# Optimization experiments

Hardware: AMD Instinct MI355X
Metric: run time of the kernel (lower is better)

Reference implementation:

```python
import jax, jax.numpy as jnp
import numpy as np

CONF_THRESH = 0.01
TOP_K = 200
NMS_THRESH = 0.45


def setup_inputs() -> dict:
    key = jax.random.key(0)
    k1, k2, k3, k4, k5 = jax.random.split(key, 5)
    B, N, C = 32, 8732, 21
    return {
        "loc_data": jax.random.normal(k1, (B, N, 4), jnp.float32),
        "conf_data": jax.random.normal(k2, (B, N, C), jnp.float32),
        "loc_data2": jax.random.normal(k3, (B, N, 4), jnp.float32),
        "conf_data2": jax.random.normal(k4, (B, N, C), jnp.float32),
        "dbox_list": jax.random.uniform(k5, (N, 4), jnp.float32),
    }


def decode(loc, dbox):
    # SSD decode with variances (0.1, 0.2); loc,dbox: [N,4]; returns xyxy
    cxcy = dbox[:, :2] + loc[:, :2] * 0.1 * dbox[:, 2:]
    wh = dbox[:, 2:] * jnp.exp(loc[:, 2:] * 0.2)
    return jnp.concatenate([cxcy - wh * 0.5, cxcy + wh * 0.5], axis=-1)


def iou_matrix(b):
    # b: [K,4] xyxy -> [K,K] IoU
    x1 = jnp.maximum(b[:, None, 0], b[None, :, 0])
    y1 = jnp.maximum(b[:, None, 1], b[None, :, 1])
    x2 = jnp.minimum(b[:, None, 2], b[None, :, 2])
    y2 = jnp.minimum(b[:, None, 3], b[None, :, 3])
    inter = jnp.clip(x2 - x1, 0.0) * jnp.clip(y2 - y1, 0.0)
    area = (b[:, 2] - b[:, 0]) * (b[:, 3] - b[:, 1])
    union = area[:, None] + area[None, :] - inter
    return inter / union


def nms_class(scores, boxes):
    # scores: [M], boxes: [M,4] for one (image, class)
    masked = jnp.where(scores > CONF_THRESH, scores, -1.0)  # drop sub-threshold
    cand_s, idx = jax.lax.top_k(masked, TOP_K)              # top_k candidate pool
    cand_b = boxes[idx]
    valid = cand_s > CONF_THRESH
    iou = iou_matrix(cand_b)

    def step(suppressed, j):
        keep_j = valid[j] & (~suppressed[j])
        suppressed = suppressed | (keep_j & (iou[j] > NMS_THRESH))
        return suppressed, keep_j

    _, keep = jax.lax.scan(step, jnp.zeros((TOP_K,), bool), jnp.arange(TOP_K))
    entries = jnp.concatenate([cand_s[:, None], cand_b], axis=1)  # [K,5] = (score, box)
    pos = jnp.cumsum(keep) - 1
    pos = jnp.where(keep, pos, TOP_K)  # out-of-bounds -> dropped
    return jnp.zeros((TOP_K, 5), entries.dtype).at[pos].set(entries, mode="drop")


def reference(loc_data, conf_data, loc_data2, conf_data2, dbox_list):
    B, N, _ = loc_data.shape
    C = conf_data.shape[2]
    conf = jax.nn.softmax(conf_data, axis=-1)    # [B,N,C]
    conf2 = jax.nn.softmax(conf_data2, axis=-1)
    boxes1 = jax.vmap(decode, in_axes=(0, None))(loc_data, dbox_list)   # [B,N,4]
    boxes2 = jax.vmap(decode, in_axes=(0, None))(loc_data2, dbox_list)
    # horizontal flip of second (TTA) view: x1' = 1 - x2, x2' = 1 - x1
    boxes2 = jnp.stack(
        [1.0 - boxes2[..., 2], boxes2[..., 1], 1.0 - boxes2[..., 0], boxes2[..., 3]],
        axis=-1,
    )
    boxes = jnp.concatenate([boxes1, boxes2], axis=1)   # [B,2N,4]
    scores = jnp.concatenate([conf, conf2], axis=1)     # [B,2N,C]
    scores = jnp.moveaxis(scores, -1, 1)                # [B,C,2N]
    # vmap over batch and (non-background) classes
    per_class = jax.vmap(jax.vmap(nms_class, in_axes=(0, None)), in_axes=(0, 0))(
        scores[:, 1:], boxes
    )  # [B,C-1,TOP_K,5]
    out = jnp.zeros((B, C, TOP_K, 5), loc_data.dtype)
    return out.at[:, 1:].set(per_class)
```

## Files before the change

### kernel.cpp

```cpp
#include <hip/hip_runtime.h>

#define B_ 32
#define N_ 8732
#define N2_ 17464
#define N4_ 4366
#define C_ 21
#define NCLS 20
#define K_ 200
#define CONF_T 0.01f
#define NMS_T 0.45f
#define TPB_S 256
#define TPB_N 512
#define POOL 1024
#define RANKCAP 512
#define HB 1024

typedef unsigned long long u64;
typedef unsigned int u32;

__global__ __launch_bounds__(TPB_S) void softmax_kernel(
    const float* __restrict__ conf1, const float* __restrict__ conf2,
    float* __restrict__ scores)
{
  __shared__ float lds[TPB_S * C_];
  const int t = threadIdx.x;
  const int tile = blockIdx.x * TPB_S;
  const int b = blockIdx.y;
  const int view = blockIdx.z;
  int cnt = N_ - tile; if (cnt > TPB_S) cnt = TPB_S;
  const float* conf = view ? conf2 : conf1;
  const float4* src = (const float4*)(conf + ((size_t)b * N_ + tile) * C_);
  float4* l4 = (float4*)lds;
  const int n4 = (cnt * C_) >> 2;
  for (int i = t; i < n4; i += TPB_S) l4[i] = src[i];
  __syncthreads();
  if (t < cnt) {
    float x[C_];
#pragma unroll
    for (int i = 0; i < C_; ++i) x[i] = lds[t * C_ + i];
    float m = x[0];
#pragma unroll
    for (int i = 1; i < C_; ++i) m = fmaxf(m, x[i]);
    float e[C_];
    float sum = 0.0f;
#pragma unroll
    for (int i = 0; i < C_; ++i) { e[i] = __expf(x[i] - m); sum += e[i]; }
    float inv = 1.0f / sum;
    float* o = scores + ((size_t)b * NCLS) * N2_ + (size_t)view * N_ + (tile + t);
#pragma unroll
    for (int c = 1; c < C_; ++c) { *o = e[c] * inv; o += N2_; }
  }
}

__global__ __launch_bounds__(TPB_N, 2) void nms_kernel(
    const float* __restrict__ scores,
    const float4* __restrict__ loc1,
    const float4* __restrict__ loc2,
    const float4* __restrict__ dbox,
    float* __restrict__ out)
{
  const int t = threadIdx.x;
  const int lane = t & 63;
  const int wv = t >> 6;
  const int bimg = blockIdx.x / NCLS;
  const int cls = 1 + (blockIdx.x % NCLS);
  const float4* sc4 = (const float4*)(scores + ((size_t)bimg * NCLS + (cls - 1)) * N2_);
  float* ob = out + ((size_t)bimg * C_ + cls) * K_ * 5;

  __shared__ u32 hist[HB];
  __shared__ u64 pool[POOL] __attribute__((aligned(16)));
  __shared__ u64 spool[256];
  __shared__ float4 bb[K_];
  __shared__ float bar[K_];
  __shared__ u64 rowmask[K_][4];
  __shared__ u64 validmask[4];
  __shared__ u32 wtot[8];
  __shared__ u32 sh_sel, sh_Sb, sh_Sn, sh_nc;

  {
    const float4 z4 = make_float4(0.f, 0.f, 0.f, 0.f);
    if (t < 250) ((float4*)ob)[t] = z4;
    if (cls == 1 && t >= 256 && t < 506)
      ((float4*)(out + (size_t)bimg * C_ * K_ * 5))[t - 256] = z4;
  }

  float4 v[9];
#pragma unroll
  for (int k = 0; k < 9; ++k) {
    int i = t + k * TPB_N;
    v[k] = (i < N4_) ? sc4[i] : make_float4(0.f, 0.f, 0.f, 0.f);
  }

  hist[t] = 0u;
  pool[t] = 0ULL; pool[t + TPB_N] = 0ULL;
  if (t == 0) sh_nc = 0u;
  __syncthreads();

  {
    const int hb = wv << 6;
#pragma unroll
    for (int k = 0; k < 9; ++k) {
      float ss[4] = {v[k].x, v[k].y, v[k].z, v[k].w};
#pragma unroll
      for (int c2 = 0; c2 < 4; ++c2) {
        float s = ss[c2];
        if (s > CONF_T)
          atomicAdd(&hist[hb + ((__float_as_uint(s) >> 20) - 960u)], 1u);
      }
    }
  }
  __syncthreads();

  if (t < 64) {
    u32 c = hist[t]       + hist[t + 64]  + hist[t + 128] + hist[t + 192]
          + hist[t + 256] + hist[t + 320] + hist[t + 384] + hist[t + 448];
    u32 x = c;
#pragma unroll
    for (int off = 1; off < 64; off <<= 1) {
      u32 y = __shfl_down(x, off);
      if (lane + off < 64) x += y;
    }
    u32 total = __shfl(x, 0);
    u32 Sn = x - c;
    if (total < (u32)K_) {
      if (t == 0) sh_sel = 0xFFFFFFFFu;
    } else if (x >= (u32)K_ && Sn < (u32)K_) {
      sh_sel = (u32)t; sh_Sb = x; sh_Sn = Sn;
    }
  }
  __syncthreads();

  u32 loKey, prefix = 0, Gacc = 0;
  bool needMore = false;
  if (sh_sel == 0xFFFFFFFFu) {
    loKey = 1u;
  } else {
    prefix = sh_sel + 960u;
    loKey = prefix << 20;
    Gacc = sh_Sn;
    needMore = sh_Sb > (u32)RANKCAP;
  }

  for (int lvl = 1; lvl <= 2 && needMore; ++lvl) {
    const int shift = (lvl == 1) ? 10 : 0;
    const int mshift = shift + 10;
    for (int h = t; h < HB; h += TPB_N) hist[h] = 0u;
    __syncthreads();
#pragma unroll
    for (int k = 0; k < 9; ++k) {
      float ss[4] = {v[k].x, v[k].y, v[k].z, v[k].w};
#pragma unroll
      for (int c2 = 0; c2 < 4; ++c2) {
        float s = ss[c2];
        if (s > CONF_T) {
          u32 key = __float_as_uint(s);
          if ((key >> mshift) == prefix)
            atomicAdd(&hist[(key >> shift) & (HB - 1)], 1u);
        }
      }
    }
    __syncthreads();
    u32 c0 = hist[2 * t], c1 = hist[2 * t + 1];
    u32 T = c0 + c1;
    u32 x = T;
#pragma unroll
    for (int off = 1; off < 64; off <<= 1) {
      u32 y = __shfl_down(x, off);
      if (lane + off < 64) x += y;
    }
    if (lane == 0) wtot[wv] = x;
    __syncthreads();
    u32 wafter = 0;
    for (int w = wv + 1; w < 8; ++w) wafter += wtot[w];
    u32 after_me = (x - T) + wafter;
    u32 S1 = c1 + after_me, S0 = c0 + S1;
    hist[2 * t] = S0; hist[2 * t + 1] = S1;
    __syncthreads();
    u32 need = (u32)K_ - Gacc;
    for (int h = t; h < HB; h += TPB_N) {
      u32 Sb = hist[h];
      u32 Sn2 = (h + 1 < HB) ? hist[h + 1] : 0u;
      if (Sb >= need && Sn2 < need) { sh_sel = (u32)h; sh_Sb = Sb; sh_Sn = Sn2; }
    }
    __syncthreads();
    prefix = (prefix << 10) | sh_sel;
    u32 candTotal = Gacc + sh_Sb;
    Gacc += sh_Sn;
    loKey = prefix << shift;
    needMore = (candTotal > (u32)RANKCAP) && (lvl < 2);
  }

#pragma unroll
  for (int k = 0; k < 9; ++k) {
    int i = t + k * TPB_N;
    float ss[4] = {v[k].x, v[k].y, v[k].z, v[k].w};
#pragma unroll
    for (int c2 = 0; c2 < 4; ++c2) {
      float s = ss[c2];
      u32 key = __float_as_uint(s);
      bool pred = (s > CONF_T) && (key >= loKey);
      u64 bal = __ballot(pred);
      if (bal) {
        u32 wb = 0;
        if (lane == 0) wb = atomicAdd(&sh_nc, (u32)__popcll(bal));
        wb = __shfl(wb, 0);
        if (pred) {
          u32 pos = wb + (u32)__popcll(bal & ((1ULL << lane) - 1ULL));
          if (pos < (u32)POOL)
            pool[pos] = ((u64)key << 32) | (u64)(0xFFFFFFFFu - (u32)(i * 4 + c2));
        }
      }
    }
  }
  __syncthreads();

  u32 nc = sh_nc < (u32)POOL ? sh_nc : (u32)POOL;
  if (t < 256) spool[t] = 0ULL;
  const bool dual = nc > (u32)TPB_N;
  u64 my0 = (t < (int)nc) ? pool[t] : 0ULL;
  u64 my1 = (dual && t + TPB_N < (int)nc) ? pool[t + TPB_N] : 0ULL;
  __syncthreads();
  u32 r0 = 0, r1 = 0;
  if ((u32)(t & ~63) < nc) {
    if (!dual) {
#pragma unroll 4
      for (u32 k = 0; k < nc; k += 2) {
        ulonglong2 pk = *(const ulonglong2*)&pool[k];
        r0 += (pk.x > my0) ? 1u : 0u;
        r0 += (pk.y > my0) ? 1u : 0u;
      }
    } else {
#pragma unroll 4
      for (u32 k = 0; k < nc; k += 2) {
        ulonglong2 pk = *(const ulonglong2*)&pool[k];
        r0 += (pk.x > my0) ? 1u : 0u;
        r0 += (pk.y > my0) ? 1u : 0u;
        r1 += (pk.x > my1) ? 1u : 0u;
        r1 += (pk.y > my1) ? 1u : 0u;
      }
    }
  }
  if (my0 != 0ULL && r0 < (u32)K_) spool[r0] = my0;
  if (dual && my1 != 0ULL && r1 < (u32)K_) spool[r1] = my1;
  __syncthreads();

  float scv = 0.f;
  if (t < K_) {
    float x1 = 0.f, y1 = 0.f, x2 = 0.f, y2 = 0.f, area = 0.f;
    u64 e = spool[t];
    u32 kb = (u32)(e >> 32);
    if (kb != 0u) {
      scv = __uint_as_float(kb);
      u32 idx = 0xFFFFFFFFu - (u32)(e & 0xFFFFFFFFu);
      int nn = (idx < (u32)N_) ? (int)idx : (int)(idx - N_);
      float4 l = (idx < (u32)N_) ? loc1[(size_t)bimg * N_ + nn]
                                 : loc2[(size_t)bimg * N_ + nn];
      float4 d = dbox[nn];
      float cx = d.x + l.x * 0.1f * d.z;
      float cy = d.y + l.y * 0.1f * d.w;
      float w = d.z * __expf(l.z * 0.2f);
      float h = d.w * __expf(l.w * 0.2f);
      x1 = cx - w * 0.5f; y1 = cy - h * 0.5f;
      x2 = cx + w * 0.5f; y2 = cy + h * 0.5f;
      if (idx >= (u32)N_) {
        float tmp = 1.0f - x2; x2 = 1.0f - x1; x1 = tmp;
      }
      area = (x2 - x1) * (y2 - y1);
    }
    bb[t] = make_float4(x1, y1, x2, y2);
    bar[t] = area;
  } else if (t >= 256) {
    for (int i = t - 256; i < 4 * K_; i += 256) ((u64*)rowmask)[i] = 0ULL;
  }
  {
    bool myvalid = (t < K_) && (scv > CONF_T);
    u64 bal = __ballot(myvalid);
    if (lane == 0 && wv < 4) validmask[wv] = bal;
  }
  __syncthreads();

  if (t < 2 * K_) {
    const int j = (t < K_) ? t : (t - K_);
    const int h = (t < K_) ? 0 : 1;
    const int L = K_ - 1 - j;
    const int half = (L + 1) >> 1;
    const int s0c = j + 1 + (h ? half : 0);
    const int e0c = h ? K_ : (j + 1 + half);
    if (s0c < e0c) {
      float4 mb = bb[j];
      float ma = bar[j];
      for (int w = (s0c >> 6); w <= ((e0c - 1) >> 6); ++w) {
        int ka = (w << 6) > s0c ? (w << 6) : s0c;
        int kb2 = ((w + 1) << 6) < e0c ? ((w + 1) << 6) : e0c;
        u64 m = 0ULL;
        for (int k2 = ka; k2 < kb2; ++k2) {
          float4 obx = bb[k2];
          float ox1 = fmaxf(mb.x, obx.x);
          float oy1 = fmaxf(mb.y, obx.y);
          float ox2 = fminf(mb.z, obx.z);
          float oy2 = fminf(mb.w, obx.w);
          float inter = fmaxf(ox2 - ox1, 0.f) * fmaxf(oy2 - oy1, 0.f);
          float uni = ma + bar[k2] - inter;
          m |= (inter > NMS_T * uni) ? (1ULL << (k2 & 63)) : 0ULL;
        }
        if (m) atomicOr(&rowmask[j][w], m);
      }
    }
  }
  __syncthreads();

  if (t < 64) {
    const u64 vv0 = validmask[0], vv1 = validmask[1];
    const u64 vv2 = validmask[2], vv3 = validmask[3];
    u64 s0 = 0, s1 = 0, s2 = 0, s3 = 0;
    u64 k0 = 0, k1 = 0, k2m = 0, k3 = 0;
#pragma unroll 8
    for (int j = 0; j < 64; ++j) {
      u64 q0 = rowmask[j][0], q1 = rowmask[j][1], q2 = rowmask[j][2], q3 = rowmask[j][3];
      u64 bit = 1ULL << j;
      if ((vv0 & bit) && !(s0 & bit)) { s0 |= q0; s1 |= q1; s2 |= q2; s3 |= q3; k0 |= bit; }
    }
#pragma unroll 8
    for (int j = 64; j < 128; ++j) {
      u64 q1 = rowmask[j][1], q2 = rowmask[j][2], q3 = rowmask[j][3];
      u64 bit = 1ULL << (j & 63);
      if ((vv1 & bit) && !(s1 & bit)) { s1 |= q1; s2 |= q2; s3 |= q3; k1 |= bit; }
    }
#pragma unroll 8
    for (int j = 128; j < 192; ++j) {
      u64 q2 = rowmask[j][2], q3 = rowmask[j][3];
      u64 bit = 1ULL << (j & 63);
      if ((vv2 & bit) && !(s2 & bit)) { s2 |= q2; s3 |= q3; k2m |= bit; }
    }
#pragma unroll
    for (int j = 192; j < K_; ++j) {
      u64 q3 = rowmask[j][3];
      u64 bit = 1ULL << (j & 63);
      if ((vv3 & bit) && !(s3 & bit)) { s3 |= q3; k3 |= bit; }
    }
    const u32 n0 = (u32)__popcll(k0);
    const u32 n01 = n0 + (u32)__popcll(k1);
    const u32 n012 = n01 + (u32)__popcll(k2m);
    const u64 below = (1ULL << lane) - 1ULL;
#pragma unroll
    for (int w = 0; w < 4; ++w) {
      int j = (w << 6) + lane;
      if (j < K_) {
        u64 kw = (w == 0) ? k0 : (w == 1) ? k1 : (w == 2) ? k2m : k3;
        if ((kw >> lane) & 1ULL) {
          int pos2 = (int)__popcll(kw & below)
                  + (int)((w == 0) ? 0u : (w == 1) ? n0 : (w == 2) ? n01 : n012);
          u64 e = spool[j];
          float sc = __uint_as_float((u32)(e >> 32));
          float4 bx = bb[j];
          float* o = ob + (size_t)pos2 * 5;
          o[0] = sc; o[1] = bx.x; o[2] = bx.y; o[3] = bx.z; o[4] = bx.w;
        }
      }
    }
  }
}

extern "C" void kernel_launch(void* const* d_in, const int* in_sizes, int n_in,
                              void* d_out, int out_size, void* d_ws, size_t ws_size,
                              hipStream_t stream) {
  const float* loc1 = (const float*)d_in[0];
  const float* conf1 = (const float*)d_in[1];
  const float* loc2 = (const float*)d_in[2];
  const float* conf2 = (const float*)d_in[3];
  const float* dbox = (const float*)d_in[4];
  float* out = (float*)d_out;
  float* scores = (float*)d_ws;

  dim3 g1((N_ + TPB_S - 1) / TPB_S, B_, 2);
  softmax_kernel<<<g1, TPB_S, 0, stream>>>(conf1, conf2, scores);

  nms_kernel<<<B_ * NCLS, TPB_N, 0, stream>>>(
      scores, (const float4*)loc1, (const float4*)loc2, (const float4*)dbox, out);
}
```

Before: 157.0 us.

## Store softmax max/inv-sum only and recompute class scores inside NMS kernel

The first kernel now writes only a per-box (max, 1/sum) pair instead of the full 20-class transposed probability array. The NMS kernel reads the raw logits for its class with a stride of C, applies exp and scale itself, and uses the shared denominators. Blocks are reordered so consecutive blocks handle the same class across images, which changes the cache access pattern. This cuts the intermediate workspace write and read traffic, but NMS blocks now make strided, uncoalesced gathers and compute extra exps per element.

```diff
diff --git a/kernel.cpp b/kernel.cpp
--- a/kernel.cpp
+++ b/kernel.cpp
@@ -18,9 +18,9 @@
 typedef unsigned long long u64;
 typedef unsigned int u32;
 
-__global__ __launch_bounds__(TPB_S) void softmax_kernel(
+__global__ __launch_bounds__(TPB_S) void denom_kernel(
     const float* __restrict__ conf1, const float* __restrict__ conf2,
-    float* __restrict__ scores)
+    float2* __restrict__ denom)
 {
   __shared__ float lds[TPB_S * C_];
   const int t = threadIdx.x;
@@ -41,19 +41,18 @@
     float m = x[0];
 #pragma unroll
     for (int i = 1; i < C_; ++i) m = fmaxf(m, x[i]);
-    float e[C_];
     float sum = 0.0f;
 #pragma unroll
-    for (int i = 0; i < C_; ++i) { e[i] = __expf(x[i] - m); sum += e[i]; }
+    for (int i = 0; i < C_; ++i) sum += __expf(x[i] - m);
     float inv = 1.0f / sum;
-    float* o = scores + ((size_t)b * NCLS) * N2_ + (size_t)view * N_ + (tile + t);
-#pragma unroll
-    for (int c = 1; c < C_; ++c) { *o = e[c] * inv; o += N2_; }
+    denom[(size_t)b * N2_ + (size_t)view * N_ + tile + t] = make_float2(m, inv);
   }
 }
 
 __global__ __launch_bounds__(TPB_N, 2) void nms_kernel(
-    const float* __restrict__ scores,
+    const float* __restrict__ conf1,
+    const float* __restrict__ conf2,
+    const float2* __restrict__ denom,
     const float4* __restrict__ loc1,
     const float4* __restrict__ loc2,
     const float4* __restrict__ dbox,
@@ -62,9 +61,8 @@
   const int t = threadIdx.x;
   const int lane = t & 63;
   const int wv = t >> 6;
-  const int bimg = blockIdx.x / NCLS;
-  const int cls = 1 + (blockIdx.x % NCLS);
-  const float4* sc4 = (const float4*)(scores + ((size_t)bimg * NCLS + (cls - 1)) * N2_);
+  const int bimg = blockIdx.x & 31;
+  const int cls = 1 + (blockIdx.x >> 5);
   float* ob = out + ((size_t)bimg * C_ + cls) * K_ * 5;
 
   __shared__ u32 hist[HB];
@@ -88,7 +86,22 @@
 #pragma unroll
   for (int k = 0; k < 9; ++k) {
     int i = t + k * TPB_N;
-    v[k] = (i < N4_) ? sc4[i] : make_float4(0.f, 0.f, 0.f, 0.f);
+    if (i < N4_) {
+      const int a0 = i << 2;
+      const float* cb = (a0 < N_)
+        ? conf1 + ((size_t)bimg * N_ + a0) * C_ + cls
+        : conf2 + ((size_t)bimg * N_ + (a0 - N_)) * C_ + cls;
+      const float s0 = cb[0], s1 = cb[C_], s2 = cb[2 * C_], s3 = cb[3 * C_];
+      const float2* dd = denom + (size_t)bimg * N2_ + a0;
+      const float4 dA = *(const float4*)dd;
+      const float4 dB = *(const float4*)(dd + 2);
+      v[k].x = __expf(s0 - dA.x) * dA.y;
+      v[k].y = __expf(s1 - dA.z) * dA.w;
+      v[k].z = __expf(s2 - dB.x) * dB.y;
+      v[k].w = __expf(s3 - dB.z) * dB.w;
+    } else {
+      v[k] = make_float4(0.f, 0.f, 0.f, 0.f);
+    }
   }
 
   hist[t] = 0u;
@@ -370,11 +383,12 @@
   const float* conf2 = (const float*)d_in[3];
   const float* dbox = (const float*)d_in[4];
   float* out = (float*)d_out;
-  float* scores = (float*)d_ws;
+  float2* denom = (float2*)d_ws;
 
   dim3 g1((N_ + TPB_S - 1) / TPB_S, B_, 2);
-  softmax_kernel<<<g1, TPB_S, 0, stream>>>(conf1, conf2, scores);
+  denom_kernel<<<g1, TPB_S, 0, stream>>>(conf1, conf2, denom);
 
   nms_kernel<<<B_ * NCLS, TPB_N, 0, stream>>>(
-      scores, (const float4*)loc1, (const float4*)loc2, (const float4*)dbox, out);
+      conf1, conf2, denom, (const float4*)loc1, (const float4*)loc2,
+      (const float4*)dbox, out);
 }
```

Result: slower. 198.3 us (+26.3%).

## Use finer 2048-bin first-level radix histogram for top-k threshold selection

Applied to the files above, without the earlier changes.

Replaces the per-wave 64-bin coarse histogram with a single 2048-bin histogram on the top 17 key bits, then adjusts the refinement levels to 10 and 5 bits. The finer first pass is meant to narrow the candidate bin enough that the costly re-histogram passes over all scores are usually skipped. In exchange it needs a block-wide prefix scan over 2048 bins, more LDS, and possibly more atomic contention on shared bins.

```diff
diff --git a/kernel.cpp b/kernel.cpp
--- a/kernel.cpp
+++ b/kernel.cpp
@@ -13,7 +13,9 @@
 #define TPB_N 512
 #define POOL 1024
 #define RANKCAP 512
+#define HB0 2048
 #define HB 1024
+#define BIN0 30791u
 
 typedef unsigned long long u64;
 typedef unsigned int u32;
@@ -67,7 +69,7 @@
   const float4* sc4 = (const float4*)(scores + ((size_t)bimg * NCLS + (cls - 1)) * N2_);
   float* ob = out + ((size_t)bimg * C_ + cls) * K_ * 5;
 
-  __shared__ u32 hist[HB];
+  __shared__ u32 hist[HB0];
   __shared__ u64 pool[POOL] __attribute__((aligned(16)));
   __shared__ u64 spool[256];
   __shared__ float4 bb[K_];
@@ -91,59 +93,68 @@
     v[k] = (i < N4_) ? sc4[i] : make_float4(0.f, 0.f, 0.f, 0.f);
   }
 
-  hist[t] = 0u;
+  hist[t] = 0u; hist[t + 512] = 0u; hist[t + 1024] = 0u; hist[t + 1536] = 0u;
   pool[t] = 0ULL; pool[t + TPB_N] = 0ULL;
   if (t == 0) sh_nc = 0u;
   __syncthreads();
 
+#pragma unroll
+  for (int k = 0; k < 9; ++k) {
+    float ss[4] = {v[k].x, v[k].y, v[k].z, v[k].w};
+#pragma unroll
+    for (int c2 = 0; c2 < 4; ++c2) {
+      float s = ss[c2];
+      if (s > CONF_T)
+        atomicAdd(&hist[(__float_as_uint(s) >> 15) - BIN0], 1u);
+    }
+  }
+  __syncthreads();
+
   {
-    const int hb = wv << 6;
-#pragma unroll
-    for (int k = 0; k < 9; ++k) {
-      float ss[4] = {v[k].x, v[k].y, v[k].z, v[k].w};
-#pragma unroll
-      for (int c2 = 0; c2 < 4; ++c2) {
-        float s = ss[c2];
-        if (s > CONF_T)
-          atomicAdd(&hist[hb + ((__float_as_uint(s) >> 20) - 960u)], 1u);
-      }
-    }
-  }
-  __syncthreads();
-
-  if (t < 64) {
-    u32 c = hist[t]       + hist[t + 64]  + hist[t + 128] + hist[t + 192]
-          + hist[t + 256] + hist[t + 320] + hist[t + 384] + hist[t + 448];
-    u32 x = c;
+    u32 c0 = hist[4 * t + 0], c1 = hist[4 * t + 1];
+    u32 c2b = hist[4 * t + 2], c3 = hist[4 * t + 3];
+    u32 T = c0 + c1 + c2b + c3;
+    u32 x = T;
 #pragma unroll
     for (int off = 1; off < 64; off <<= 1) {
       u32 y = __shfl_down(x, off);
       if (lane + off < 64) x += y;
     }
-    u32 total = __shfl(x, 0);
-    u32 Sn = x - c;
-    if (total < (u32)K_) {
-      if (t == 0) sh_sel = 0xFFFFFFFFu;
-    } else if (x >= (u32)K_ && Sn < (u32)K_) {
-      sh_sel = (u32)t; sh_Sb = x; sh_Sn = Sn;
-    }
+    if (lane == 0) wtot[wv] = x;
+    __syncthreads();
+    u32 wafter = 0;
+    for (int w = wv + 1; w < 8; ++w) wafter += wtot[w];
+    u32 after_me = (x - T) + wafter;
+    u32 S3 = c3 + after_me, S2 = c2b + S3, S1 = c1 + S2, S0 = c0 + S1;
+    hist[4 * t + 0] = S0; hist[4 * t + 1] = S1;
+    hist[4 * t + 2] = S2; hist[4 * t + 3] = S3;
   }
   __syncthreads();
 
   u32 loKey, prefix = 0, Gacc = 0;
   bool needMore = false;
-  if (sh_sel == 0xFFFFFFFFu) {
-    loKey = 1u;
-  } else {
-    prefix = sh_sel + 960u;
-    loKey = prefix << 20;
-    Gacc = sh_Sn;
-    needMore = sh_Sb > (u32)RANKCAP;
+  {
+    u32 total = hist[0];
+    if (total < (u32)K_) {
+      loKey = 1u;
+    } else {
+      for (int h = t; h < HB0; h += TPB_N) {
+        u32 Sb = hist[h];
+        u32 Sn = (h + 1 < HB0) ? hist[h + 1] : 0u;
+        if (Sb >= (u32)K_ && Sn < (u32)K_) { sh_sel = (u32)h; sh_Sb = Sb; sh_Sn = Sn; }
+      }
+      __syncthreads();
+      prefix = sh_sel + BIN0;
+      loKey = prefix << 15;
+      Gacc = sh_Sn;
+      needMore = sh_Sb > (u32)RANKCAP;
+    }
   }
 
   for (int lvl = 1; lvl <= 2 && needMore; ++lvl) {
-    const int shift = (lvl == 1) ? 10 : 0;
-    const int mshift = shift + 10;
+    const int shift = (lvl == 1) ? 5 : 0;
+    const int mshift = (lvl == 1) ? 15 : 5;
+    const u32 bmask = (lvl == 1) ? 1023u : 31u;
     for (int h = t; h < HB; h += TPB_N) hist[h] = 0u;
     __syncthreads();
 #pragma unroll
@@ -155,7 +166,7 @@
         if (s > CONF_T) {
           u32 key = __float_as_uint(s);
           if ((key >> mshift) == prefix)
-            atomicAdd(&hist[(key >> shift) & (HB - 1)], 1u);
+            atomicAdd(&hist[(key >> shift) & bmask], 1u);
         }
       }
     }
@@ -183,7 +194,7 @@
       if (Sb >= need && Sn2 < need) { sh_sel = (u32)h; sh_Sb = Sb; sh_Sn = Sn2; }
     }
     __syncthreads();
-    prefix = (prefix << 10) | sh_sel;
+    prefix = (prefix << ((lvl == 1) ? 10 : 5)) | sh_sel;
     u32 candTotal = Gacc + sh_Sb;
     Gacc += sh_Sn;
     loKey = prefix << shift;
```

After: 151.6 us. -3.5%, faster.
